# Performance work log

Hardware: AMD Instinct MI355X
Metric: run time of the kernel (lower is better)

The kernel has to match this reference:

```python
import jax, jax.numpy as jnp
import numpy as np

NX = 768
N_HEAD = 12
N_CTX = 2048
MASKED_BIAS = -10000.0


def setup_inputs() -> dict:
    key = jax.random.key(0)
    ks = jax.random.split(key, 6)
    bs, seq = 2, N_CTX
    hidden_states = jax.random.normal(ks[0], (bs, seq, NX), dtype=jnp.float32)
    attention_mask = jnp.zeros((bs, 1, 1, seq), dtype=jnp.float32)
    # Conv1D params: out = x @ W + b, W: (in, out)
    w_attn = jax.random.normal(ks[1], (NX, 3 * NX), dtype=jnp.float32) * 0.02
    b_attn = jnp.zeros((3 * NX,), dtype=jnp.float32)
    w_proj = jax.random.normal(ks[2], (NX, NX), dtype=jnp.float32) * 0.02
    b_proj = jnp.zeros((NX,), dtype=jnp.float32)
    return {
        "hidden_states": hidden_states,
        "attention_mask": attention_mask,
        "w_attn": w_attn,
        "b_attn": b_attn,
        "w_proj": w_proj,
        "b_proj": b_proj,
    }


def reference(hidden_states, attention_mask, w_attn, b_attn, w_proj, b_proj):
    bs, seq, _ = hidden_states.shape
    hd = NX // N_HEAD  # 64
    qkv = hidden_states @ w_attn + b_attn  # [bs, seq, 3*nx]
    query, key, value = jnp.split(qkv, 3, axis=2)
    # Faithful to source: direct reshape (NOT standard split-heads transpose)
    q = query.reshape(bs, N_HEAD, seq, hd)
    k = key.reshape(bs, N_HEAD, seq, hd)
    v = value.reshape(bs, N_HEAD, seq, hd)
    w = jnp.einsum("bhqd,bhkd->bhqk", q, k) / jnp.sqrt(jnp.float32(hd))
    # causal mask: tril, sliced as bias[:, :, ns-nd:ns, :ns] with nd=ns=seq
    mask = jnp.tril(jnp.ones((seq, seq), dtype=jnp.float32))[None, None]
    w = w * mask + MASKED_BIAS * (1.0 - mask)
    w = w + attention_mask
    w = jax.nn.softmax(w, axis=-1)  # dropout = identity (eval mode)
    a = jnp.einsum("bhqk,bhkd->bhqd", w, v)
    a = a.transpose(0, 2, 1, 3).reshape(bs, seq, NX)
    a = a @ w_proj + b_proj  # resid dropout = identity
    return a
```

## Files before the change

kernel.cpp:

```cpp
#include <hip/hip_runtime.h>
#include <hip/hip_bf16.h>

typedef unsigned short u16;
typedef short bf16x8 __attribute__((ext_vector_type(8)));
typedef float f32x4 __attribute__((ext_vector_type(4)));

#define NXC 768
#define NHEAD 12
#define SEQ 2048
#define BSZ 2
#define HD 64
#define NCHUNK 40
#define LOG2E 1.4426950408889634f

__device__ inline u16 f2bf(float f) {
    unsigned int u = __float_as_uint(f);
    unsigned int r = u + 0x7fffu + ((u >> 16) & 1u);
    return (u16)(r >> 16);
}
__device__ inline float ex2(float x) { return __builtin_amdgcn_exp2f(x); }

__global__ void cast4_kernel(const float* __restrict__ in, u16* __restrict__ out, int n4) {
    int i = blockIdx.x * 256 + threadIdx.x;
    if (i >= n4) return;
    float4 v = ((const float4*)in)[i];
    ushort4 o;
    o.x = f2bf(v.x); o.y = f2bf(v.y); o.z = f2bf(v.z); o.w = f2bf(v.w);
    ((ushort4*)out)[i] = o;
}

__global__ void transpose_cast_kernel(const float* __restrict__ in, u16* __restrict__ out,
                                      int R, int C) {
    __shared__ float tile[32][33];
    int cb = blockIdx.x * 32, rb = blockIdx.y * 32;
    int tx = threadIdx.x, ty = threadIdx.y;
    #pragma unroll
    for (int i = 0; i < 32; i += 8)
        tile[ty + i][tx] = in[(size_t)(rb + ty + i) * C + cb + tx];
    __syncthreads();
    #pragma unroll
    for (int i = 0; i < 32; i += 8)
        out[(size_t)(cb + ty + i) * R + rb + tx] = f2bf(tile[tx][ty + i]);
}

__global__ __launch_bounds__(256) void vt_kernel(const u16* __restrict__ Vb,
                                                 u16* __restrict__ Vtg) {
    __shared__ u16 tile[64][68];
    int y = blockIdx.y;
    size_t base = (size_t)y * (SEQ * HD);
    int ss0 = blockIdx.x * 64;
    int t = threadIdx.x;
    #pragma unroll
    for (int c = t; c < 512; c += 256) {
        int r = c >> 3, col = (c & 7) * 8;
        *(uint4*)&tile[r][col] = *(const uint4*)&Vb[base + (size_t)(ss0 + r) * HD + col];
    }
    __syncthreads();
    #pragma unroll
    for (int c = t; c < 512; c += 256) {
        int dd = c >> 3, s8 = (c & 7) * 8;
        ushort4 a, bq;
        a.x = tile[s8 + 0][dd]; a.y = tile[s8 + 1][dd];
        a.z = tile[s8 + 2][dd]; a.w = tile[s8 + 3][dd];
        bq.x = tile[s8 + 4][dd]; bq.y = tile[s8 + 5][dd];
        bq.z = tile[s8 + 6][dd]; bq.w = tile[s8 + 7][dd];
        u16* dst = &Vtg[base + (size_t)dd * SEQ + ss0 + s8];
        *(ushort4*)dst = a;
        *(ushort4*)(dst + 4) = bq;
    }
}

template <int EPI>
__global__ __launch_bounds__(256) void gemm_bt_kernel(
    const u16* __restrict__ A, const u16* __restrict__ BT,
    const float* __restrict__ bias,
    u16* __restrict__ outQ, u16* __restrict__ outK, u16* __restrict__ outV,
    float* __restrict__ outF,
    int M, int N, int K) {
    __shared__ u16 As[128 * 32];
    __shared__ u16 Bs[64 * 32];
    int tileM = blockIdx.y * 128, tileN = blockIdx.x * 64;
    int t = threadIdx.x;
    int lane = t & 63, wave = t >> 6;
    int wm = wave * 32;
    int quad = lane >> 4, l16 = lane & 15;
    f32x4 acc[2][4] = {};

    int r0 = t >> 2, c0 = (t & 3) * 8;
    const u16* Ag0 = A + (size_t)(tileM + r0) * K + c0;
    const u16* Ag1 = Ag0 + (size_t)64 * K;
    const u16* Bg0 = BT + (size_t)(tileN + r0) * K + c0;
    u16* AsW0 = &As[r0 * 32 + c0];
    u16* AsW1 = &As[(r0 + 64) * 32 + c0];
    u16* BsW0 = &Bs[(r0 & 63) * 32 + c0];

    uint4 ra0 = *(const uint4*)(Ag0);
    uint4 ra1 = *(const uint4*)(Ag1);
    uint4 rb0 = *(const uint4*)(Bg0);

    for (int k0 = 0; k0 < K; k0 += 32) {
        __syncthreads();
        *(uint4*)AsW0 = ra0;
        *(uint4*)AsW1 = ra1;
        *(uint4*)BsW0 = rb0;
        __syncthreads();
        if (k0 + 32 < K) {
            ra0 = *(const uint4*)(Ag0 + k0 + 32);
            ra1 = *(const uint4*)(Ag1 + k0 + 32);
            rb0 = *(const uint4*)(Bg0 + k0 + 32);
        }
        bf16x8 af[2], bfr[4];
        #pragma unroll
        for (int i = 0; i < 2; ++i)
            af[i] = *(const bf16x8*)&As[(wm + i * 16 + l16) * 32 + quad * 8];
        #pragma unroll
        for (int j = 0; j < 4; ++j)
            bfr[j] = *(const bf16x8*)&Bs[(j * 16 + l16) * 32 + quad * 8];
        #pragma unroll
        for (int i = 0; i < 2; ++i)
            #pragma unroll
            for (int j = 0; j < 4; ++j)
                acc[i][j] = __builtin_amdgcn_mfma_f32_16x16x32_bf16(af[i], bfr[j], acc[i][j], 0, 0, 0);
    }

    #pragma unroll
    for (int i = 0; i < 2; ++i) {
        #pragma unroll
        for (int j = 0; j < 4; ++j) {
            int n = tileN + j * 16 + l16;
            float bv = bias[n];
            #pragma unroll
            for (int r = 0; r < 4; ++r) {
                int m = tileM + wm + i * 16 + quad * 4 + r;
                float v = acc[i][j][r] + bv;
                if (EPI == 0) {
                    if (n < 768) {
                        outQ[(size_t)m * 768 + n] = f2bf(v);
                    } else if (n < 1536) {
                        outK[(size_t)m * 768 + (n - 768)] = f2bf(v * (0.125f * LOG2E));
                    } else {
                        outV[(size_t)m * 768 + (n - 1536)] = f2bf(v);
                    }
                } else {
                    outF[(size_t)m * N + n] = v;
                }
            }
        }
    }
}

__global__ __launch_bounds__(512) void attn_mfma_kernel(
    const u16* __restrict__ Q, const u16* __restrict__ Kg,
    const u16* __restrict__ Vtg, const float* __restrict__ amask,
    u16* __restrict__ Opart, float* __restrict__ Lpart) {
    __shared__ u16 Ks[64][72];
    __shared__ u16 Vt[64][72];
    __shared__ u16 Ps[8][16][72];
    __shared__ float Ams[64];

    int bh = blockIdx.y;
    int b = bh / NHEAD, h = bh % NHEAD;
    int p = NCHUNK - 1 - (int)blockIdx.x;
    int bx = 15, c = 0, a = 0;
    #pragma unroll
    for (int i = 0; i < 16; ++i) {
        int n = (i >> 2) + 1;
        if (p < a + n) { bx = i; c = p - a; break; }
        a += n;
    }
    int kbase = c * 512;
    int nt = 2 * (bx + 1) - 8 * c;
    if (nt > 8) nt = 8;

    int t = threadIdx.x;
    int w = t >> 6, lane = t & 63;
    int quad = lane >> 4, l16 = lane & 15;
    size_t headbase = (size_t)b * (SEQ * NXC) + (size_t)h * (SEQ * HD);
    size_t headbaseT = (size_t)(b * NHEAD + h) * (SEQ * HD);

    int r0 = bx * 128;
    int qw0 = r0 + w * 16;
    int qrow = qw0 + l16;
    bf16x8 qf[2];
    #pragma unroll
    for (int s = 0; s < 2; ++s)
        qf[s] = *(const bf16x8*)&Q[headbase + (size_t)(qw0 + l16) * HD + s * 32 + quad * 8];

    float l_part = 0.f;
    f32x4 o[4] = {};

    int pr_row = t >> 3, pr_col = (t & 7) * 8;
    uint4 kr, vr; float amr;
    {
        int k0 = kbase;
        kr = *(const uint4*)&Kg[headbase + (size_t)(k0 + pr_row) * HD + pr_col];
        vr = *(const uint4*)&Vtg[headbaseT + (size_t)pr_row * SEQ + k0 + pr_col];
        if (t < 64) amr = amask[(size_t)b * SEQ + k0 + t];
    }

    for (int kt = 0; kt < nt; ++kt) {
        int k0 = kbase + kt * 64;
        __syncthreads();
        *(uint4*)&Ks[pr_row][pr_col] = kr;
        *(uint4*)&Vt[pr_row][pr_col] = vr;
        if (t < 64) Ams[t] = amr * LOG2E;
        __syncthreads();
        if (kt + 1 < nt) {
            int kn = k0 + 64;
            kr = *(const uint4*)&Kg[headbase + (size_t)(kn + pr_row) * HD + pr_col];
            vr = *(const uint4*)&Vtg[headbaseT + (size_t)pr_row * SEQ + kn + pr_col];
            if (t < 64) amr = amask[(size_t)b * SEQ + kn + t];
        }

        if (k0 > qw0 + 15) continue;

        bf16x8 kf[2][4];
        #pragma unroll
        for (int s = 0; s < 2; ++s)
            #pragma unroll
            for (int j = 0; j < 4; ++j)
                kf[s][j] = *(const bf16x8*)&Ks[j * 16 + l16][s * 32 + quad * 8];
        float amv[4][4];
        #pragma unroll
        for (int j = 0; j < 4; ++j)
            #pragma unroll
            for (int r = 0; r < 4; ++r)
                amv[j][r] = Ams[j * 16 + quad * 4 + r];

        f32x4 sacc[4] = {};
        #pragma unroll
        for (int s = 0; s < 2; ++s)
            #pragma unroll
            for (int j = 0; j < 4; ++j)
                sacc[j] = __builtin_amdgcn_mfma_f32_16x16x32_bf16(kf[s][j], qf[s], sacc[j], 0, 0, 0);

        bool diag = (k0 + 63 > qw0);
        #pragma unroll
        for (int j = 0; j < 4; ++j) {
            float pv[4];
            #pragma unroll
            for (int r = 0; r < 4; ++r) {
                float pp = ex2(sacc[j][r] + amv[j][r]);
                if (diag && (k0 + j * 16 + quad * 4 + r > qrow)) pp = 0.f;
                pv[r] = pp;
            }
            l_part += (pv[0] + pv[1]) + (pv[2] + pv[3]);
            unsigned pk01 = ((__float_as_uint(pv[0]) + 0x8000u) >> 16) |
                            ((__float_as_uint(pv[1]) + 0x8000u) & 0xffff0000u);
            unsigned pk23 = ((__float_as_uint(pv[2]) + 0x8000u) >> 16) |
                            ((__float_as_uint(pv[3]) + 0x8000u) & 0xffff0000u);
            *(uint2*)&Ps[w][l16][j * 16 + quad * 4] = make_uint2(pk01, pk23);
        }

        #pragma unroll
        for (int s = 0; s < 2; ++s) {
            bf16x8 pf = *(const bf16x8*)&Ps[w][l16][s * 32 + quad * 8];
            #pragma unroll
            for (int dc = 0; dc < 4; ++dc) {
                bf16x8 vf = *(const bf16x8*)&Vt[dc * 16 + l16][s * 32 + quad * 8];
                o[dc] = __builtin_amdgcn_mfma_f32_16x16x32_bf16(pf, vf, o[dc], 0, 0, 0);
            }
        }
    }

    float l = l_part + __shfl_xor(l_part, 16);
    l += __shfl_xor(l, 32);
    u16* Ob = Opart + ((size_t)bh * NCHUNK + p) * (128 * 64);
    float* Lb = Lpart + ((size_t)bh * NCHUNK + p) * 128;
    #pragma unroll
    for (int dc = 0; dc < 4; ++dc)
        #pragma unroll
        for (int r = 0; r < 4; ++r) {
            int rl = w * 16 + quad * 4 + r;
            Ob[rl * 64 + dc * 16 + l16] = f2bf(o[dc][r]);
        }
    if (quad == 0) Lb[w * 16 + l16] = l;
}

__global__ __launch_bounds__(256) void attn_combine_kernel(
    const u16* __restrict__ Opart, const float* __restrict__ Lpart,
    u16* __restrict__ Aout) {
    __shared__ float winv[32];
    int bh = blockIdx.y;
    int b = bh / NHEAD, h = bh % NHEAD;
    int row0 = blockIdx.x * 32;
    int bx = row0 >> 7;
    int g = bx >> 2;
    int nch = g + 1;
    int p0 = 2 * g * (g + 1) + (bx & 3) * (g + 1);
    int rbase = row0 & 127;
    int t = threadIdx.x;

    if (t < 32) {
        float L = 0.f;
        for (int c = 0; c < nch; ++c)
            L += Lpart[((size_t)bh * NCHUNK + p0 + c) * 128 + rbase + t];
        winv[t] = 1.0f / L;
    }
    __syncthreads();

    int row = t >> 3;
    int d0 = (t & 7) * 8;
    int rl = rbase + row;
    float acc[8] = {};
    for (int c = 0; c < nch; ++c) {
        uint4 u = *(const uint4*)&Opart[(((size_t)bh * NCHUNK + p0 + c) * 128 + rl) * 64 + d0];
        acc[0] += __uint_as_float(u.x << 16);
        acc[1] += __uint_as_float(u.x & 0xffff0000u);
        acc[2] += __uint_as_float(u.y << 16);
        acc[3] += __uint_as_float(u.y & 0xffff0000u);
        acc[4] += __uint_as_float(u.z << 16);
        acc[5] += __uint_as_float(u.z & 0xffff0000u);
        acc[6] += __uint_as_float(u.w << 16);
        acc[7] += __uint_as_float(u.w & 0xffff0000u);
    }
    float s = winv[row];
    uint4 o;
    o.x = (unsigned)f2bf(acc[0] * s) | ((unsigned)f2bf(acc[1] * s) << 16);
    o.y = (unsigned)f2bf(acc[2] * s) | ((unsigned)f2bf(acc[3] * s) << 16);
    o.z = (unsigned)f2bf(acc[4] * s) | ((unsigned)f2bf(acc[5] * s) << 16);
    o.w = (unsigned)f2bf(acc[6] * s) | ((unsigned)f2bf(acc[7] * s) << 16);
    *(uint4*)&Aout[((size_t)b * SEQ + row0 + row) * NXC + h * HD + d0] = o;
}

extern "C" void kernel_launch(void* const* d_in, const int* in_sizes, int n_in,
                              void* d_out, int out_size, void* d_ws, size_t ws_size,
                              hipStream_t stream) {
    const float* hs     = (const float*)d_in[0];
    const float* amask  = (const float*)d_in[1];
    const float* w_attn = (const float*)d_in[2];
    const float* b_attn = (const float*)d_in[3];
    const float* w_proj = (const float*)d_in[4];
    const float* b_proj = (const float*)d_in[5];
    float* out = (float*)d_out;

    const int M = BSZ * SEQ;
    char* ws = (char*)d_ws;
    auto alloc = [&](size_t bytes) {
        char* p = ws;
        ws += (bytes + 255) & ~(size_t)255;
        return p;
    };
    u16* HSbf   = (u16*)alloc((size_t)M * NXC * 2);
    u16* WaT    = (u16*)alloc((size_t)3 * NXC * NXC * 2);
    u16* WpT    = (u16*)alloc((size_t)NXC * NXC * 2);
    u16* Qb     = (u16*)alloc((size_t)M * NXC * 2);
    u16* Kb     = (u16*)alloc((size_t)M * NXC * 2);
    u16* Vb     = (u16*)alloc((size_t)M * NXC * 2);
    u16* Vtg    = (u16*)alloc((size_t)M * NXC * 2);
    u16* Ab     = (u16*)alloc((size_t)M * NXC * 2);
    u16* Opart  = (u16*)alloc((size_t)BSZ * NHEAD * NCHUNK * 128 * 64 * 2);
    float* Lpart = (float*)alloc((size_t)BSZ * NHEAD * NCHUNK * 128 * 4);

    {
        int n4 = M * NXC / 4;
        cast4_kernel<<<dim3((n4 + 255) / 256), dim3(256), 0, stream>>>(hs, HSbf, n4);
        transpose_cast_kernel<<<dim3(3 * NXC / 32, NXC / 32), dim3(32, 8), 0, stream>>>(w_attn, WaT, NXC, 3 * NXC);
        transpose_cast_kernel<<<dim3(NXC / 32, NXC / 32), dim3(32, 8), 0, stream>>>(w_proj, WpT, NXC, NXC);
    }
    gemm_bt_kernel<0><<<dim3(3 * NXC / 64, M / 128), dim3(256), 0, stream>>>(
        HSbf, WaT, b_attn, Qb, Kb, Vb, nullptr, M, 3 * NXC, NXC);
    vt_kernel<<<dim3(SEQ / 64, BSZ * NHEAD), dim3(256), 0, stream>>>(Vb, Vtg);
    attn_mfma_kernel<<<dim3(NCHUNK, BSZ * NHEAD), dim3(512), 0, stream>>>(
        Qb, Kb, Vtg, amask, Opart, Lpart);
    attn_combine_kernel<<<dim3(SEQ / 32, BSZ * NHEAD), dim3(256), 0, stream>>>(
        Opart, Lpart, Ab);
    gemm_bt_kernel<1><<<dim3(NXC / 64, M / 128), dim3(256), 0, stream>>>(
        Ab, WpT, b_proj, nullptr, nullptr, nullptr, out, M, NXC, NXC);
}
```

Measured before the change: 175.0 us.

## Fuse hidden-state bf16 cast into QKV GEMM and give attention waves two row groups

The separate fp32-to-bf16 cast kernel for hidden states is removed, and the QKV GEMM now loads fp32 directly and converts in registers. This drops one launch and a round trip through an intermediate buffer, at the cost of reading fp32 data (twice the bytes) in the GEMM A-operand loads. The attention kernel moves from 512 to 256 threads, with each wave handling 32 query rows as two 16-row groups. This reuses each K/V fragment loaded from LDS across two MFMA groups, but it raises register pressure and halves the waves per block.

```diff
diff --git a/kernel.cpp b/kernel.cpp
--- a/kernel.cpp
+++ b/kernel.cpp
@@ -18,16 +18,18 @@
     unsigned int r = u + 0x7fffu + ((u >> 16) & 1u);
     return (u16)(r >> 16);
 }
+__device__ inline unsigned pk2(float lo, float hi) {
+    return (unsigned)f2bf(lo) | ((unsigned)f2bf(hi) << 16);
+}
+__device__ inline uint4 ldcvt(const float* p) {
+    float4 a = *(const float4*)p;
+    float4 b = *(const float4*)(p + 4);
+    uint4 o;
+    o.x = pk2(a.x, a.y); o.y = pk2(a.z, a.w);
+    o.z = pk2(b.x, b.y); o.w = pk2(b.z, b.w);
+    return o;
+}
 __device__ inline float ex2(float x) { return __builtin_amdgcn_exp2f(x); }
-
-__global__ void cast4_kernel(const float* __restrict__ in, u16* __restrict__ out, int n4) {
-    int i = blockIdx.x * 256 + threadIdx.x;
-    if (i >= n4) return;
-    float4 v = ((const float4*)in)[i];
-    ushort4 o;
-    o.x = f2bf(v.x); o.y = f2bf(v.y); o.z = f2bf(v.z); o.w = f2bf(v.w);
-    ((ushort4*)out)[i] = o;
-}
 
 __global__ void transpose_cast_kernel(const float* __restrict__ in, u16* __restrict__ out,
                                       int R, int C) {
@@ -72,7 +74,7 @@
 
 template <int EPI>
 __global__ __launch_bounds__(256) void gemm_bt_kernel(
-    const u16* __restrict__ A, const u16* __restrict__ BT,
+    const void* __restrict__ Av, const u16* __restrict__ BT,
     const float* __restrict__ bias,
     u16* __restrict__ outQ, u16* __restrict__ outK, u16* __restrict__ outV,
     float* __restrict__ outF,
@@ -87,16 +89,19 @@
     f32x4 acc[2][4] = {};
 
     int r0 = t >> 2, c0 = (t & 3) * 8;
-    const u16* Ag0 = A + (size_t)(tileM + r0) * K + c0;
-    const u16* Ag1 = Ag0 + (size_t)64 * K;
+    const float* Af0 = (const float*)Av + (size_t)(tileM + r0) * K + c0;
+    const float* Af1 = Af0 + (size_t)64 * K;
+    const u16*   Ab0 = (const u16*)Av + (size_t)(tileM + r0) * K + c0;
+    const u16*   Ab1 = Ab0 + (size_t)64 * K;
     const u16* Bg0 = BT + (size_t)(tileN + r0) * K + c0;
     u16* AsW0 = &As[r0 * 32 + c0];
     u16* AsW1 = &As[(r0 + 64) * 32 + c0];
     u16* BsW0 = &Bs[(r0 & 63) * 32 + c0];
 
-    uint4 ra0 = *(const uint4*)(Ag0);
-    uint4 ra1 = *(const uint4*)(Ag1);
-    uint4 rb0 = *(const uint4*)(Bg0);
+    uint4 ra0, ra1, rb0;
+    if (EPI == 0) { ra0 = ldcvt(Af0); ra1 = ldcvt(Af1); }
+    else          { ra0 = *(const uint4*)(Ab0); ra1 = *(const uint4*)(Ab1); }
+    rb0 = *(const uint4*)(Bg0);
 
     for (int k0 = 0; k0 < K; k0 += 32) {
         __syncthreads();
@@ -105,8 +110,8 @@
         *(uint4*)BsW0 = rb0;
         __syncthreads();
         if (k0 + 32 < K) {
-            ra0 = *(const uint4*)(Ag0 + k0 + 32);
-            ra1 = *(const uint4*)(Ag1 + k0 + 32);
+            if (EPI == 0) { ra0 = ldcvt(Af0 + k0 + 32); ra1 = ldcvt(Af1 + k0 + 32); }
+            else          { ra0 = *(const uint4*)(Ab0 + k0 + 32); ra1 = *(const uint4*)(Ab1 + k0 + 32); }
             rb0 = *(const uint4*)(Bg0 + k0 + 32);
         }
         bf16x8 af[2], bfr[4];
@@ -149,13 +154,13 @@
     }
 }
 
-__global__ __launch_bounds__(512) void attn_mfma_kernel(
+__global__ __launch_bounds__(256) void attn_mfma_kernel(
     const u16* __restrict__ Q, const u16* __restrict__ Kg,
     const u16* __restrict__ Vtg, const float* __restrict__ amask,
     u16* __restrict__ Opart, float* __restrict__ Lpart) {
     __shared__ u16 Ks[64][72];
     __shared__ u16 Vt[64][72];
-    __shared__ u16 Ps[8][16][72];
+    __shared__ u16 Ps[4][2][16][72];
     __shared__ float Ams[64];
 
     int bh = blockIdx.y;
@@ -179,40 +184,48 @@
     size_t headbaseT = (size_t)(b * NHEAD + h) * (SEQ * HD);
 
     int r0 = bx * 128;
-    int qw0 = r0 + w * 16;
-    int qrow = qw0 + l16;
-    bf16x8 qf[2];
-    #pragma unroll
-    for (int s = 0; s < 2; ++s)
-        qf[s] = *(const bf16x8*)&Q[headbase + (size_t)(qw0 + l16) * HD + s * 32 + quad * 8];
-
-    float l_part = 0.f;
-    f32x4 o[4] = {};
+    int qw0 = r0 + w * 32;
+    bf16x8 qf[2][2];
+    #pragma unroll
+    for (int g = 0; g < 2; ++g)
+        #pragma unroll
+        for (int s = 0; s < 2; ++s)
+            qf[g][s] = *(const bf16x8*)&Q[headbase + (size_t)(qw0 + g * 16 + l16) * HD + s * 32 + quad * 8];
+
+    float l_part[2] = {0.f, 0.f};
+    f32x4 o[2][4] = {};
 
     int pr_row = t >> 3, pr_col = (t & 7) * 8;
-    uint4 kr, vr; float amr;
+    uint4 kr0, kr1, vr0, vr1; float amr;
     {
         int k0 = kbase;
-        kr = *(const uint4*)&Kg[headbase + (size_t)(k0 + pr_row) * HD + pr_col];
-        vr = *(const uint4*)&Vtg[headbaseT + (size_t)pr_row * SEQ + k0 + pr_col];
+        kr0 = *(const uint4*)&Kg[headbase + (size_t)(k0 + pr_row) * HD + pr_col];
+        kr1 = *(const uint4*)&Kg[headbase + (size_t)(k0 + pr_row + 32) * HD + pr_col];
+        vr0 = *(const uint4*)&Vtg[headbaseT + (size_t)pr_row * SEQ + k0 + pr_col];
+        vr1 = *(const uint4*)&Vtg[headbaseT + (size_t)(pr_row + 32) * SEQ + k0 + pr_col];
         if (t < 64) amr = amask[(size_t)b * SEQ + k0 + t];
     }
 
     for (int kt = 0; kt < nt; ++kt) {
         int k0 = kbase + kt * 64;
         __syncthreads();
-        *(uint4*)&Ks[pr_row][pr_col] = kr;
-        *(uint4*)&Vt[pr_row][pr_col] = vr;
+        *(uint4*)&Ks[pr_row][pr_col] = kr0;
+        *(uint4*)&Ks[pr_row + 32][pr_col] = kr1;
+        *(uint4*)&Vt[pr_row][pr_col] = vr0;
+        *(uint4*)&Vt[pr_row + 32][pr_col] = vr1;
         if (t < 64) Ams[t] = amr * LOG2E;
         __syncthreads();
         if (kt + 1 < nt) {
             int kn = k0 + 64;
-            kr = *(const uint4*)&Kg[headbase + (size_t)(kn + pr_row) * HD + pr_col];
-            vr = *(const uint4*)&Vtg[headbaseT + (size_t)pr_row * SEQ + kn + pr_col];
+            kr0 = *(const uint4*)&Kg[headbase + (size_t)(kn + pr_row) * HD + pr_col];
+            kr1 = *(const uint4*)&Kg[headbase + (size_t)(kn + pr_row + 32) * HD + pr_col];
+            vr0 = *(const uint4*)&Vtg[headbaseT + (size_t)pr_row * SEQ + kn + pr_col];
+            vr1 = *(const uint4*)&Vtg[headbaseT + (size_t)(pr_row + 32) * SEQ + kn + pr_col];
             if (t < 64) amr = amask[(size_t)b * SEQ + kn + t];
         }
 
-        if (k0 > qw0 + 15) continue;
+        if (k0 > qw0 + 31) continue;
+        bool act0 = (k0 <= qw0 + 15);
 
         bf16x8 kf[2][4];
         #pragma unroll
@@ -220,61 +233,72 @@
             #pragma unroll
             for (int j = 0; j < 4; ++j)
                 kf[s][j] = *(const bf16x8*)&Ks[j * 16 + l16][s * 32 + quad * 8];
-        float amv[4][4];
+        float4 am4[4];
         #pragma unroll
         for (int j = 0; j < 4; ++j)
-            #pragma unroll
-            for (int r = 0; r < 4; ++r)
-                amv[j][r] = Ams[j * 16 + quad * 4 + r];
-
-        f32x4 sacc[4] = {};
-        #pragma unroll
-        for (int s = 0; s < 2; ++s)
-            #pragma unroll
-            for (int j = 0; j < 4; ++j)
-                sacc[j] = __builtin_amdgcn_mfma_f32_16x16x32_bf16(kf[s][j], qf[s], sacc[j], 0, 0, 0);
-
-        bool diag = (k0 + 63 > qw0);
-        #pragma unroll
-        for (int j = 0; j < 4; ++j) {
-            float pv[4];
-            #pragma unroll
-            for (int r = 0; r < 4; ++r) {
-                float pp = ex2(sacc[j][r] + amv[j][r]);
-                if (diag && (k0 + j * 16 + quad * 4 + r > qrow)) pp = 0.f;
-                pv[r] = pp;
+            am4[j] = *(const float4*)&Ams[j * 16 + quad * 4];
+
+        #pragma unroll
+        for (int g = 0; g < 2; ++g) {
+            if (g == 0 && !act0) continue;
+            int qg0 = qw0 + g * 16;
+            int qrow = qg0 + l16;
+            f32x4 sacc[4] = {};
+            #pragma unroll
+            for (int s = 0; s < 2; ++s)
+                #pragma unroll
+                for (int j = 0; j < 4; ++j)
+                    sacc[j] = __builtin_amdgcn_mfma_f32_16x16x32_bf16(kf[s][j], qf[g][s], sacc[j], 0, 0, 0);
+
+            bool diag = (k0 + 63 > qg0);
+            #pragma unroll
+            for (int j = 0; j < 4; ++j) {
+                float pv[4];
+                float am[4] = {am4[j].x, am4[j].y, am4[j].z, am4[j].w};
+                #pragma unroll
+                for (int r = 0; r < 4; ++r) {
+                    float pp = ex2(sacc[j][r] + am[r]);
+                    if (diag && (k0 + j * 16 + quad * 4 + r > qrow)) pp = 0.f;
+                    pv[r] = pp;
+                }
+                l_part[g] += (pv[0] + pv[1]) + (pv[2] + pv[3]);
+                unsigned pk01 = ((__float_as_uint(pv[0]) + 0x8000u) >> 16) |
+                                ((__float_as_uint(pv[1]) + 0x8000u) & 0xffff0000u);
+                unsigned pk23 = ((__float_as_uint(pv[2]) + 0x8000u) >> 16) |
+                                ((__float_as_uint(pv[3]) + 0x8000u) & 0xffff0000u);
+                *(uint2*)&Ps[w][g][l16][j * 16 + quad * 4] = make_uint2(pk01, pk23);
             }
-            l_part += (pv[0] + pv[1]) + (pv[2] + pv[3]);
-            unsigned pk01 = ((__float_as_uint(pv[0]) + 0x8000u) >> 16) |
-                            ((__float_as_uint(pv[1]) + 0x8000u) & 0xffff0000u);
-            unsigned pk23 = ((__float_as_uint(pv[2]) + 0x8000u) >> 16) |
-                            ((__float_as_uint(pv[3]) + 0x8000u) & 0xffff0000u);
-            *(uint2*)&Ps[w][l16][j * 16 + quad * 4] = make_uint2(pk01, pk23);
         }
 
         #pragma unroll
         for (int s = 0; s < 2; ++s) {
-            bf16x8 pf = *(const bf16x8*)&Ps[w][l16][s * 32 + quad * 8];
+            bf16x8 pf1 = *(const bf16x8*)&Ps[w][1][l16][s * 32 + quad * 8];
+            bf16x8 pf0;
+            if (act0) pf0 = *(const bf16x8*)&Ps[w][0][l16][s * 32 + quad * 8];
             #pragma unroll
             for (int dc = 0; dc < 4; ++dc) {
                 bf16x8 vf = *(const bf16x8*)&Vt[dc * 16 + l16][s * 32 + quad * 8];
-                o[dc] = __builtin_amdgcn_mfma_f32_16x16x32_bf16(pf, vf, o[dc], 0, 0, 0);
+                if (act0) o[0][dc] = __builtin_amdgcn_mfma_f32_16x16x32_bf16(pf0, vf, o[0][dc], 0, 0, 0);
+                o[1][dc] = __builtin_amdgcn_mfma_f32_16x16x32_bf16(pf1, vf, o[1][dc], 0, 0, 0);
             }
         }
     }
 
-    float l = l_part + __shfl_xor(l_part, 16);
-    l += __shfl_xor(l, 32);
     u16* Ob = Opart + ((size_t)bh * NCHUNK + p) * (128 * 64);
     float* Lb = Lpart + ((size_t)bh * NCHUNK + p) * 128;
     #pragma unroll
-    for (int dc = 0; dc < 4; ++dc)
-        #pragma unroll
-        for (int r = 0; r < 4; ++r) {
-            int rl = w * 16 + quad * 4 + r;
-            Ob[rl * 64 + dc * 16 + l16] = f2bf(o[dc][r]);
-        }
-    if (quad == 0) Lb[w * 16 + l16] = l;
+    for (int g = 0; g < 2; ++g) {
+        float l = l_part[g] + __shfl_xor(l_part[g], 16);
+        l += __shfl_xor(l, 32);
+        #pragma unroll
+        for (int dc = 0; dc < 4; ++dc)
+            #pragma unroll
+            for (int r = 0; r < 4; ++r) {
+                int rl = w * 32 + g * 16 + quad * 4 + r;
+                Ob[rl * 64 + dc * 16 + l16] = f2bf(o[g][dc][r]);
+            }
+        if (quad == 0) Lb[w * 32 + g * 16 + l16] = l;
+    }
 }
 
 __global__ __launch_bounds__(256) void attn_combine_kernel(
@@ -316,10 +340,10 @@
     }
     float s = winv[row];
     uint4 o;
-    o.x = (unsigned)f2bf(acc[0] * s) | ((unsigned)f2bf(acc[1] * s) << 16);
-    o.y = (unsigned)f2bf(acc[2] * s) | ((unsigned)f2bf(acc[3] * s) << 16);
-    o.z = (unsigned)f2bf(acc[4] * s) | ((unsigned)f2bf(acc[5] * s) << 16);
-    o.w = (unsigned)f2bf(acc[6] * s) | ((unsigned)f2bf(acc[7] * s) << 16);
+    o.x = pk2(acc[0] * s, acc[1] * s);
+    o.y = pk2(acc[2] * s, acc[3] * s);
+    o.z = pk2(acc[4] * s, acc[5] * s);
+    o.w = pk2(acc[6] * s, acc[7] * s);
     *(uint4*)&Aout[((size_t)b * SEQ + row0 + row) * NXC + h * HD + d0] = o;
 }
 
@@ -341,7 +365,6 @@
         ws += (bytes + 255) & ~(size_t)255;
         return p;
     };
-    u16* HSbf   = (u16*)alloc((size_t)M * NXC * 2);
     u16* WaT    = (u16*)alloc((size_t)3 * NXC * NXC * 2);
     u16* WpT    = (u16*)alloc((size_t)NXC * NXC * 2);
     u16* Qb     = (u16*)alloc((size_t)M * NXC * 2);
@@ -352,16 +375,13 @@
     u16* Opart  = (u16*)alloc((size_t)BSZ * NHEAD * NCHUNK * 128 * 64 * 2);
     float* Lpart = (float*)alloc((size_t)BSZ * NHEAD * NCHUNK * 128 * 4);
 
-    {
-        int n4 = M * NXC / 4;
-        cast4_kernel<<<dim3((n4 + 255) / 256), dim3(256), 0, stream>>>(hs, HSbf, n4);
-        transpose_cast_kernel<<<dim3(3 * NXC / 32, NXC / 32), dim3(32, 8), 0, stream>>>(w_attn, WaT, NXC, 3 * NXC);
-        transpose_cast_kernel<<<dim3(NXC / 32, NXC / 32), dim3(32, 8), 0, stream>>>(w_proj, WpT, NXC, NXC);
-    }
+    transpose_cast_kernel<<<dim3(3 * NXC / 32, NXC / 32), dim3(32, 8), 0, stream>>>(w_attn, WaT, NXC, 3 * NXC);
+    transpose_cast_kernel<<<dim3(NXC / 32, NXC / 32), dim3(32, 8), 0, stream>>>(w_proj, WpT, NXC, NXC);
+
     gemm_bt_kernel<0><<<dim3(3 * NXC / 64, M / 128), dim3(256), 0, stream>>>(
-        HSbf, WaT, b_attn, Qb, Kb, Vb, nullptr, M, 3 * NXC, NXC);
+        hs, WaT, b_attn, Qb, Kb, Vb, nullptr, M, 3 * NXC, NXC);
     vt_kernel<<<dim3(SEQ / 64, BSZ * NHEAD), dim3(256), 0, stream>>>(Vb, Vtg);
-    attn_mfma_kernel<<<dim3(NCHUNK, BSZ * NHEAD), dim3(512), 0, stream>>>(
+    attn_mfma_kernel<<<dim3(NCHUNK, BSZ * NHEAD), dim3(256), 0, stream>>>(
         Qb, Kb, Vtg, amask, Opart, Lpart);
     attn_combine_kernel<<<dim3(SEQ / 32, BSZ * NHEAD), dim3(256), 0, stream>>>(
         Opart, Lpart, Ab);
```

Result: slower. 179.9 us (+2.8%).
